# Kernel optimization log

Measured on AMD Instinct MI355X. Metric: run time of the kernel, lower is better.

The kernel has to match this reference:

```python
import jax, jax.numpy as jnp
import numpy as np

# Nemotron-H Mamba2 mixer decoder layer (prefill path, zero initial states,
# full context lengths). Dims per init_kwargs.
B, S, H = 1, 256, 4096
NH, P, G, N, K = 128, 64, 8, 128, 4   # num_heads, head_dim, n_groups, ssm_state_size, conv_kernel
D_INNER = NH * P                      # 8192
D_STATE = G * N                       # 1024
CONV_DIM = D_INNER + 2 * D_STATE      # 10240
IN_OUT = D_INNER + CONV_DIM + NH      # 18560
EPS = 1e-6


def setup_inputs() -> dict:
    key = jax.random.key(0)
    ks = jax.random.split(key, 8)
    sc = 0.02
    return {
        "hidden_states": jax.random.normal(ks[0], (B, S, H), jnp.float32),
        "conv_state": jnp.zeros((B, CONV_DIM, K - 1), jnp.float32),
        "ssm_state": jnp.zeros((B, NH, P, N), jnp.float32),
        "norm_weight": jnp.ones((H,), jnp.float32),
        "w_in": jax.random.normal(ks[1], (IN_OUT, H), jnp.float32) * sc,
        "conv_w": jax.random.normal(ks[2], (CONV_DIM, K), jnp.float32) * 0.2,
        "conv_b": jnp.zeros((CONV_DIM,), jnp.float32),
        "A_log": jax.random.uniform(ks[3], (NH,), jnp.float32, 0.0, 1.0),
        "D_param": jax.random.normal(ks[4], (NH,), jnp.float32) * 0.1,
        "dt_bias": jax.random.normal(ks[5], (NH,), jnp.float32) * 0.1,
        "ssm_norm_weight": jnp.ones((D_INNER,), jnp.float32),
        "w_out": jax.random.normal(ks[6], (H, D_INNER), jnp.float32) * sc,
    }


def _rmsnorm(x, w, eps=EPS):
    var = jnp.mean(x * x, axis=-1, keepdims=True)
    return x * jax.lax.rsqrt(var + eps) * w


def reference(hidden_states, conv_state, ssm_state, norm_weight, w_in, conv_w,
              conv_b, A_log, D_param, dt_bias, ssm_norm_weight, w_out):
    resid = hidden_states
    h = _rmsnorm(hidden_states, norm_weight)           # pre-mixer RMSNorm
    proj = jnp.einsum('bsh,oh->bso', h, w_in)          # in_proj [B,S,18560]
    gate = proj[..., :D_INNER]
    xconv = proj[..., D_INNER:D_INNER + CONV_DIM]
    dt = proj[..., D_INNER + CONV_DIM:]                # [B,S,NH]

    # depthwise causal conv1d, initial left context = conv_state
    xc = jnp.swapaxes(xconv, 1, 2)                     # [B,CONV_DIM,S]
    xpad = jnp.concatenate([conv_state, xc], axis=-1)  # [B,CONV_DIM,S+K-1]
    conv_state_out = xpad[:, :, -(K - 1):]
    y = conv_b[None, :, None]
    for j in range(K):                                 # K=4 taps, unrolled
        y = y + conv_w[:, j][None, :, None] * xpad[:, :, j:j + S]
    y = jax.nn.silu(jnp.swapaxes(y, 1, 2))             # [B,S,CONV_DIM]

    xs = y[..., :D_INNER].reshape(B, S, NH, P)
    Bs = y[..., D_INNER:D_INNER + D_STATE].reshape(B, S, G, N)
    Cs = y[..., D_INNER + D_STATE:].reshape(B, S, G, N)

    A = -jnp.exp(A_log)                                # [NH]
    dtp = jax.nn.softplus(dt + dt_bias)                # [B,S,NH]
    rep = NH // G
    Bh = jnp.repeat(Bs, rep, axis=2)                   # [B,S,NH,N]
    Ch = jnp.repeat(Cs, rep, axis=2)

    def step(state, inp):
        x_t, b_t, c_t, dt_t = inp                      # [B,NH,P],[B,NH,N],[B,NH,N],[B,NH]
        dA = jnp.exp(dt_t * A)                         # [B,NH]
        state = state * dA[..., None, None] + (dt_t[..., None] * x_t)[..., None] * b_t[:, :, None, :]
        y_t = jnp.einsum('bhpn,bhn->bhp', state, c_t)
        return state, y_t

    inps = (jnp.swapaxes(xs, 0, 1), jnp.swapaxes(Bh, 0, 1),
            jnp.swapaxes(Ch, 0, 1), jnp.swapaxes(dtp, 0, 1))
    ssm_state_out, ys = jax.lax.scan(step, ssm_state, inps)
    ys = jnp.swapaxes(ys, 0, 1) + D_param[None, None, :, None] * xs
    ssm_out = ys.reshape(B, S, D_INNER)

    # gated grouped RMSNorm (group_size = D_INNER // G = 1024)
    gated = ssm_out * jax.nn.silu(gate)
    gsize = D_INNER // G
    gg = gated.reshape(B, S, D_INNER // gsize, gsize)
    var = jnp.mean(gg * gg, axis=-1, keepdims=True)
    normed = (gg * jax.lax.rsqrt(var + EPS)).reshape(B, S, D_INNER) * ssm_norm_weight

    out = jnp.einsum('bsd,hd->bsh', normed, w_out)     # out_proj
    return resid + out, conv_state_out, ssm_state_out
```

## Files before the change

### kernel.cpp

```cpp
#include <hip/hip_runtime.h>
#include <hip/hip_bf16.h>

#define Sq 256
#define Hd 4096
#define NH 128
#define Pd 64
#define Gg 8
#define Nn 128
#define D_INNER 8192
#define D_STATE 1024
#define CONV_DIM 10240
#define IN_OUT 18560
#define DT_COL0 18432
#define EPSI 1e-6f

typedef _Float16 f16x8 __attribute__((ext_vector_type(8)));
typedef _Float16 f16x2 __attribute__((ext_vector_type(2)));
typedef float f32x4 __attribute__((ext_vector_type(4)));

__device__ inline ushort f2h(float f) {
  _Float16 h = (_Float16)f;
  return __builtin_bit_cast(ushort, h);
}
__device__ inline float h2f(ushort u) {
  return (float)__builtin_bit_cast(_Float16, u);
}
__device__ inline ushort f2h_lo(float f, ushort hi) {
  float hf = (float)__builtin_bit_cast(_Float16, hi);
  _Float16 l = (_Float16)(f - hf);
  return __builtin_bit_cast(ushort, l);
}
__device__ inline f16x2 pkrtz(float a, float b) {
  return __builtin_bit_cast(f16x2, __builtin_amdgcn_cvt_pkrtz(a, b));
}

__global__ __launch_bounds__(256) void rmsnorm_k(const float* __restrict__ x,
                                                 const float* __restrict__ w,
                                                 ushort* __restrict__ h_hi,
                                                 ushort* __restrict__ h_lo) {
  int s = blockIdx.x, t = threadIdx.x;
  const float4* row = reinterpret_cast<const float4*>(x + (size_t)s * Hd);
  const float4* wv  = reinterpret_cast<const float4*>(w);
  float4 v[4];
  float ss = 0.f;
#pragma unroll
  for (int i = 0; i < 4; i++) {
    v[i] = row[t + i * 256];
    ss += v[i].x * v[i].x + v[i].y * v[i].y + v[i].z * v[i].z + v[i].w * v[i].w;
  }
#pragma unroll
  for (int off = 32; off > 0; off >>= 1) ss += __shfl_xor(ss, off);
  __shared__ float red[4];
  if ((t & 63) == 0) red[t >> 6] = ss;
  __syncthreads();
  ss = red[0] + red[1] + red[2] + red[3];
  float scale = rsqrtf(ss * (1.f / (float)Hd) + EPSI);
  ushort4* hh = reinterpret_cast<ushort4*>(h_hi + (size_t)s * Hd);
  ushort4* hl = reinterpret_cast<ushort4*>(h_lo + (size_t)s * Hd);
#pragma unroll
  for (int i = 0; i < 4; i++) {
    float4 wi = wv[t + i * 256];
    float f0 = v[i].x * scale * wi.x, f1 = v[i].y * scale * wi.y;
    float f2 = v[i].z * scale * wi.z, f3 = v[i].w * scale * wi.w;
    ushort4 oh, ol;
    oh.x = f2h(f0); ol.x = f2h_lo(f0, oh.x);
    oh.y = f2h(f1); ol.y = f2h_lo(f1, oh.y);
    oh.z = f2h(f2); ol.z = f2h_lo(f2, oh.z);
    oh.w = f2h(f3); ol.w = f2h_lo(f3, oh.w);
    hh[t + i * 256] = oh;
    hl[t + i * 256] = ol;
  }
}

__global__ __launch_bounds__(256) void gemm_t128(const ushort* __restrict__ A,
                                                 const float* __restrict__ B,
                                                 float* __restrict__ C0,
                                                 ushort* __restrict__ Cp,
                                                 int ldc, int K, int kLen) {
  __shared__ __align__(16) ushort As[2][128 * 32];
  __shared__ __align__(16) ushort Bs[2][128 * 32];
  int t = threadIdx.x;
  int wave = t >> 6, lane = t & 63;
  int wr = wave >> 1, wc = wave & 1;
  int frow = lane & 15, gq = lane >> 4;
  int coltile = blockIdx.x >> 1;
  int rowBase = (blockIdx.x & 1) * 128;
  int bcol = coltile * 128;
  int z = blockIdx.z;
  int kStart = z * kLen;

  int ar = t >> 2;
  int ax = (ar >> 1) & 3;
  const ushort* ApG0 = A + (size_t)(rowBase + ar) * K + kStart + ((t & 3) ^ ax) * 8;
  const ushort* ApG1 = ApG0 + (size_t)64 * K;
  char* dstA0 = (char*)&As[0][0] + wave * 1024;
  char* dstA1 = (char*)&As[0][0] + 4096 + wave * 1024;

  int brow = t >> 1, bhalf = t & 1;
  int bx = (brow >> 1) & 3;
  const float* BpG = B + (size_t)(bcol + brow) * K + kStart + bhalf * 16;
  int bslot0 = ((2 * bhalf) ^ bx) * 16;
  int bslot1 = ((2 * bhalf + 1) ^ bx) * 16;
  float4 rb[4];

  f32x4 acc[4][4] = {};
  const int NT = kLen / 32;

#define ISSUE_B(kk) { _Pragma("unroll") for (int j = 0; j < 4; ++j) \
                        rb[j] = *(const float4*)(BpG + (kk) + j * 4); }
#define DMA_A(p, kk) { \
    __builtin_amdgcn_global_load_lds( \
        (const __attribute__((address_space(1))) void*)(ApG0 + (kk)), \
        (__attribute__((address_space(3))) void*)(dstA0 + (p) * 8192), 16, 0, 0); \
    __builtin_amdgcn_global_load_lds( \
        (const __attribute__((address_space(1))) void*)(ApG1 + (kk)), \
        (__attribute__((address_space(3))) void*)(dstA1 + (p) * 8192), 16, 0, 0); }
#define WRITE_B(p) { \
    union { f16x2 h2[8]; uint4 q[2]; } u; \
    u.h2[0] = pkrtz(rb[0].x, rb[0].y); u.h2[1] = pkrtz(rb[0].z, rb[0].w); \
    u.h2[2] = pkrtz(rb[1].x, rb[1].y); u.h2[3] = pkrtz(rb[1].z, rb[1].w); \
    u.h2[4] = pkrtz(rb[2].x, rb[2].y); u.h2[5] = pkrtz(rb[2].z, rb[2].w); \
    u.h2[6] = pkrtz(rb[3].x, rb[3].y); u.h2[7] = pkrtz(rb[3].z, rb[3].w); \
    char* bb = (char*)&Bs[0][0] + (p) * 8192 + brow * 64; \
    *(uint4*)(bb + bslot0) = u.q[0]; \
    *(uint4*)(bb + bslot1) = u.q[1]; }

  ISSUE_B(0)
  DMA_A(0, 0)
  WRITE_B(0)
  __syncthreads();

  for (int i = 0; i < NT; ++i) {
    int cur = i & 1;
    if (i + 1 < NT) {
      ISSUE_B((i + 1) * 32)
      DMA_A(cur ^ 1, (i + 1) * 32)
    }
    f16x8 af[4], bf[4];
#pragma unroll
    for (int m = 0; m < 4; ++m) {
      int row = wr * 64 + m * 16 + frow;
      af[m] = *(const f16x8*)((const char*)&As[0][0] + cur * 8192 + row * 64 +
                              ((gq ^ ((row >> 1) & 3)) * 16));
    }
#pragma unroll
    for (int n = 0; n < 4; ++n) {
      int row = wc * 64 + n * 16 + frow;
      bf[n] = *(const f16x8*)((const char*)&Bs[0][0] + cur * 8192 + row * 64 +
                              ((gq ^ ((row >> 1) & 3)) * 16));
    }
#pragma unroll
    for (int m = 0; m < 4; ++m)
#pragma unroll
      for (int n = 0; n < 4; ++n)
        acc[m][n] = __builtin_amdgcn_mfma_f32_16x16x32_f16(af[m], bf[n], acc[m][n], 0, 0, 0);
    __builtin_amdgcn_sched_barrier(0);
    if (i + 1 < NT) WRITE_B(cur ^ 1)
    __syncthreads();
  }
#undef ISSUE_B
#undef DMA_A
#undef WRITE_B

  if (z == 0) {
#pragma unroll
    for (int m = 0; m < 4; ++m) {
      int row0 = rowBase + wr * 64 + m * 16 + (lane >> 4) * 4;
#pragma unroll
      for (int n = 0; n < 4; ++n) {
        int col = bcol + wc * 64 + n * 16 + frow;
#pragma unroll
        for (int r = 0; r < 4; ++r)
          C0[(size_t)(row0 + r) * ldc + col] = acc[m][n][r];
      }
    }
  } else {
    ushort* Cz = Cp + (size_t)(z - 1) * Sq * ldc;
#pragma unroll
    for (int m = 0; m < 4; ++m) {
      int row0 = rowBase + wr * 64 + m * 16 + (lane >> 4) * 4;
#pragma unroll
      for (int n = 0; n < 4; ++n) {
        int col = bcol + wc * 64 + n * 16 + frow;
#pragma unroll
        for (int r = 0; r < 4; ++r)
          Cz[(size_t)(row0 + r) * ldc + col] = f2h(acc[m][n][r]);
      }
    }
  }
}

template<int BN, bool SPLIT>
__global__ __launch_bounds__(256) void gemm_mfma(const ushort* __restrict__ A_hi,
                                                 const ushort* __restrict__ A_lo,
                                                 const float* __restrict__ B,
                                                 float* __restrict__ C,
                                                 int ldc, int K, int kLen,
                                                 int bcol0, int M) {
  constexpr int BK = 64;
  constexpr int LDA = 72;
  constexpr int N_REP = BN / 32;
  constexpr int BQN = (BN == 128) ? 8 : 4;
  __shared__ __align__(16) ushort As[64 * LDA];
  __shared__ __align__(16) ushort Bs[BN * LDA];
  __shared__ __align__(16) ushort AsL[SPLIT ? 64 * LDA : 1];
  __shared__ __align__(16) ushort BsL[SPLIT ? BN * LDA : 1];

  int t = threadIdx.x;
  int wave = t >> 6, lane = t & 63;
  int wr = wave >> 1, wc = wave & 1;
  int frow = lane & 15, fk = (lane >> 4) * 8;
  int rowBase = blockIdx.x * 64;
  int bcol = bcol0 + blockIdx.y * BN;
  int ccol = blockIdx.y * BN;
  int kStart = blockIdx.z * kLen;
  C += (size_t)blockIdx.z * M * ldc;

  int arow = t >> 2, ak = (t & 3) * 16;
  const ushort* Ap  = A_hi + (size_t)(rowBase + arow) * K + ak;
  const ushort* ApL = SPLIT ? (A_lo + (size_t)(rowBase + arow) * K + ak) : nullptr;

  int brow, bq;
  if constexpr (BN == 128) { brow = t >> 1; bq = (t & 1) * 32; }
  else                     { brow = t >> 2; bq = (t & 3) * 16; }
  const float* Bp = B + (size_t)(bcol + brow) * K + bq;

  f32x4 acc[2][N_REP] = {};
  uint4 aPre[2], aPreL[2];
  float4 bPre[BQN];

  auto loadK = [&](int kk) {
    aPre[0] = *reinterpret_cast<const uint4*>(Ap + kk);
    aPre[1] = *reinterpret_cast<const uint4*>(Ap + kk + 8);
    if constexpr (SPLIT) {
      aPreL[0] = *reinterpret_cast<const uint4*>(ApL + kk);
      aPreL[1] = *reinterpret_cast<const uint4*>(ApL + kk + 8);
    }
#pragma unroll
    for (int j = 0; j < BQN; ++j)
      bPre[j] = *reinterpret_cast<const float4*>(Bp + kk + j * 4);
  };

  loadK(kStart);
  for (int ki = 0; ki < kLen; ki += BK) {
    __syncthreads();
    *reinterpret_cast<uint4*>(&As[arow * LDA + ak])     = aPre[0];
    *reinterpret_cast<uint4*>(&As[arow * LDA + ak + 8]) = aPre[1];
    if constexpr (SPLIT) {
      *reinterpret_cast<uint4*>(&AsL[arow * LDA + ak])     = aPreL[0];
      *reinterpret_cast<uint4*>(&AsL[arow * LDA + ak + 8]) = aPreL[1];
    }
    {
      ushort hb[BQN * 4];
      ushort lb[SPLIT ? BQN * 4 : 1];
      const float* bf = reinterpret_cast<const float*>(bPre);
#pragma unroll
      for (int j = 0; j < BQN * 4; ++j) {
        hb[j] = f2h(bf[j]);
        if constexpr (SPLIT) lb[j] = f2h_lo(bf[j], hb[j]);
      }
#pragma unroll
      for (int j = 0; j < BQN / 2; ++j)
        *reinterpret_cast<uint4*>(&Bs[brow * LDA + bq + j * 8]) =
            reinterpret_cast<const uint4*>(hb)[j];
      if constexpr (SPLIT) {
#pragma unroll
        for (int j = 0; j < BQN / 2; ++j)
          *reinterpret_cast<uint4*>(&BsL[brow * LDA + bq + j * 8]) =
              reinterpret_cast<const uint4*>(lb)[j];
      }
    }
    __syncthreads();
    if (ki + BK < kLen) loadK(kStart + ki + BK);
    f16x8 af[2][2], bfv[N_REP][2];
    f16x8 afL[SPLIT ? 2 : 1][2], bfL[SPLIT ? N_REP : 1][2];
#pragma unroll
    for (int m = 0; m < 2; ++m)
#pragma unroll
      for (int kh = 0; kh < 2; ++kh) {
        af[m][kh] = *reinterpret_cast<const f16x8*>(
            &As[(wr * 32 + m * 16 + frow) * LDA + kh * 32 + fk]);
        if constexpr (SPLIT)
          afL[m][kh] = *reinterpret_cast<const f16x8*>(
              &AsL[(wr * 32 + m * 16 + frow) * LDA + kh * 32 + fk]);
      }
#pragma unroll
    for (int n = 0; n < N_REP; ++n)
#pragma unroll
      for (int kh = 0; kh < 2; ++kh) {
        bfv[n][kh] = *reinterpret_cast<const f16x8*>(
            &Bs[(wc * (BN / 2) + n * 16 + frow) * LDA + kh * 32 + fk]);
        if constexpr (SPLIT)
          bfL[n][kh] = *reinterpret_cast<const f16x8*>(
              &BsL[(wc * (BN / 2) + n * 16 + frow) * LDA + kh * 32 + fk]);
      }
#pragma unroll
    for (int kh = 0; kh < 2; ++kh)
#pragma unroll
      for (int m = 0; m < 2; ++m)
#pragma unroll
        for (int n = 0; n < N_REP; ++n) {
          acc[m][n] = __builtin_amdgcn_mfma_f32_16x16x32_f16(af[m][kh], bfv[n][kh], acc[m][n], 0, 0, 0);
          if constexpr (SPLIT) {
            acc[m][n] = __builtin_amdgcn_mfma_f32_16x16x32_f16(af[m][kh], bfL[n][kh], acc[m][n], 0, 0, 0);
            acc[m][n] = __builtin_amdgcn_mfma_f32_16x16x32_f16(afL[m][kh], bfv[n][kh], acc[m][n], 0, 0, 0);
          }
        }
  }

#pragma unroll
  for (int m = 0; m < 2; ++m) {
    int row0 = rowBase + wr * 32 + m * 16 + (lane >> 4) * 4;
#pragma unroll
    for (int n = 0; n < N_REP; ++n) {
      int col = ccol + wc * (BN / 2) + n * 16 + frow;
#pragma unroll
      for (int r = 0; r < 4; ++r)
        C[(size_t)(row0 + r) * ldc + col] = acc[m][n][r];
    }
  }
}

__global__ __launch_bounds__(256) void reduce_in_k(float* __restrict__ proj,
                                                   const ushort* __restrict__ pp) {
  int i = blockIdx.x * 256 + threadIdx.x;
  const size_t PL = (size_t)Sq * IN_OUT;
  float4 o = reinterpret_cast<const float4*>(proj)[i];
#pragma unroll
  for (int zz = 0; zz < 3; ++zz) {
    ushort4 hv = reinterpret_cast<const ushort4*>(pp + zz * PL)[i];
    o.x += h2f(hv.x); o.y += h2f(hv.y); o.z += h2f(hv.z); o.w += h2f(hv.w);
  }
  reinterpret_cast<float4*>(proj)[i] = o;
}

__global__ __launch_bounds__(256) void conv_silu_k(const float* __restrict__ proj,
                                                   const float* __restrict__ cstate,
                                                   const float* __restrict__ cw,
                                                   const float* __restrict__ cb,
                                                   float* __restrict__ y) {
  int c = blockIdx.x * 256 + threadIdx.x;
  int s = blockIdx.y;
  float acc = cb[c];
  float4 w4 = *reinterpret_cast<const float4*>(cw + c * 4);
  float wj[4] = {w4.x, w4.y, w4.z, w4.w};
#pragma unroll
  for (int j = 0; j < 4; j++) {
    int si = s + j - 3;
    float v = (si < 0) ? cstate[c * 3 + (si + 3)]
                       : proj[(size_t)si * IN_OUT + D_INNER + c];
    acc += wj[j] * v;
  }
  float sig = 1.f / (1.f + expf(-acc));
  y[(size_t)s * CONV_DIM + c] = acc * sig;
}

__global__ __launch_bounds__(256) void conv_state_out_k(const float* __restrict__ proj,
                                                        float* __restrict__ out1) {
  int idx = blockIdx.x * 256 + threadIdx.x;
  int c = idx / 3, tt = idx % 3;
  out1[idx] = proj[(size_t)(Sq - 3 + tt) * IN_OUT + D_INNER + c];
}

__global__ __launch_bounds__(256) void dt_k(const float* __restrict__ dtfix,
                                            const float* __restrict__ dt_bias,
                                            float* __restrict__ dtp) {
  int idx = blockIdx.x * 256 + threadIdx.x;
  int hh = idx & 127;
  float v = dtfix[idx] + dtfix[32768 + idx] + dtfix[65536 + idx] + dtfix[98304 + idx]
            + dt_bias[hh];
  dtp[idx] = (v > 20.f) ? v : log1pf(expf(v));
}

#define CS 16
__global__ __launch_bounds__(256) void ssm_scan_k(const float* __restrict__ y_conv,
                                                  const float* __restrict__ dtp,
                                                  const float* __restrict__ sstate_in,
                                                  const float* __restrict__ A_log,
                                                  const float* __restrict__ D_param,
                                                  float* __restrict__ ys_out,
                                                  float* __restrict__ sstate_out) {
  int h = blockIdx.x >> 1;
  int pb = (blockIdx.x & 1) * 32;
  int t = threadIdx.x;
  int ng = t & 7, pl = t >> 3;
  int g = h >> 4;
  float A = -expf(A_log[h]);
  float Dp = D_param[h];

  float st[16];
  {
    const float* sp = sstate_in + ((size_t)h * Pd + pb + pl) * Nn + ng * 16;
#pragma unroll
    for (int i = 0; i < 16; i += 4) {
      float4 v = *reinterpret_cast<const float4*>(sp + i);
      st[i] = v.x; st[i + 1] = v.y; st[i + 2] = v.z; st[i + 3] = v.w;
    }
  }

  __shared__ float ybuf[CS][296];
  __shared__ float dts[CS];
  int lr = t >> 4;
  int lc = t & 15;

  for (int ch = 0; ch < Sq / CS; ++ch) {
    int s0 = ch * CS;
    __syncthreads();
    const float* rowp = y_conv + (size_t)(s0 + lr) * CONV_DIM;
#pragma unroll
    for (int j = 0; j < 5; ++j) {
      int c = lc + 16 * j;
      if (c < 72) {
        const float* src;
        if (c < 8)       src = rowp + h * 64 + pb + c * 4;
        else if (c < 40) src = rowp + D_INNER + g * 128 + (c - 8) * 4;
        else             src = rowp + D_INNER + D_STATE + g * 128 + (c - 40) * 4;
        *reinterpret_cast<float4*>(&ybuf[lr][c * 4]) = *reinterpret_cast<const float4*>(src);
      }
    }
    if (t < CS) dts[t] = dtp[(s0 + t) * NH + h];
    __syncthreads();

#pragma unroll 4
    for (int stp = 0; stp < CS; ++stp) {
      float dt = dts[stp];
      float dA = expf(dt * A);
      float x0 = ybuf[stp][pl];
      float dtx = dt * x0;
      float y0 = 0.f;
#pragma unroll
      for (int i = 0; i < 16; ++i) {
        float b = ybuf[stp][32 + ng * 16 + i];
        float c = ybuf[stp][160 + ng * 16 + i];
        st[i] = st[i] * dA + dtx * b;
        y0 += st[i] * c;
      }
      y0 += __shfl_xor(y0, 1); y0 += __shfl_xor(y0, 2); y0 += __shfl_xor(y0, 4);
      if (ng == 0)
        ys_out[(size_t)(s0 + stp) * D_INNER + h * 64 + pb + pl] = y0 + Dp * x0;
    }
  }

  float* so = sstate_out + ((size_t)h * Pd + pb + pl) * Nn + ng * 16;
#pragma unroll
  for (int i = 0; i < 16; i += 4)
    *reinterpret_cast<float4*>(so + i) = make_float4(st[i], st[i + 1], st[i + 2], st[i + 3]);
}

__global__ __launch_bounds__(256) void gated_norm_k(const float* __restrict__ ys,
                                                    const float* __restrict__ proj,
                                                    const float* __restrict__ w,
                                                    ushort* __restrict__ out_h) {
  int s = blockIdx.x, g = blockIdx.y, t = threadIdx.x;
  float vals[4];
  float ss = 0.f;
#pragma unroll
  for (int i = 0; i < 4; i++) {
    int d = g * 1024 + i * 256 + t;
    float gate = proj[(size_t)s * IN_OUT + d];
    float v = ys[(size_t)s * D_INNER + d] * (gate / (1.f + expf(-gate)));
    vals[i] = v;
    ss += v * v;
  }
#pragma unroll
  for (int off = 32; off > 0; off >>= 1) ss += __shfl_xor(ss, off);
  __shared__ float red[4];
  if ((t & 63) == 0) red[t >> 6] = ss;
  __syncthreads();
  ss = red[0] + red[1] + red[2] + red[3];
  float scale = rsqrtf(ss * (1.f / 1024.f) + EPSI);
#pragma unroll
  for (int i = 0; i < 4; i++) {
    int d = g * 1024 + i * 256 + t;
    out_h[(size_t)s * D_INNER + d] = f2h(vals[i] * scale * w[d]);
  }
}

__global__ __launch_bounds__(256) void reduce_out_k(const float* __restrict__ p0,
                                                    const ushort* __restrict__ pph,
                                                    const float* __restrict__ hidden,
                                                    float* __restrict__ out0) {
  int i = blockIdx.x * 256 + threadIdx.x;
  const size_t PL = (size_t)Sq * Hd;
  float4 o = reinterpret_cast<const float4*>(hidden)[i];
  float4 a = reinterpret_cast<const float4*>(p0)[i];
  o.x += a.x; o.y += a.y; o.z += a.z; o.w += a.w;
#pragma unroll
  for (int zz = 0; zz < 15; ++zz) {
    ushort4 hv = reinterpret_cast<const ushort4*>(pph + zz * PL)[i];
    o.x += h2f(hv.x); o.y += h2f(hv.y); o.z += h2f(hv.z); o.w += h2f(hv.w);
  }
  reinterpret_cast<float4*>(out0)[i] = o;
}

extern "C" void kernel_launch(void* const* d_in, const int* in_sizes, int n_in,
                              void* d_out, int out_size, void* d_ws, size_t ws_size,
                              hipStream_t stream) {
  const float* hidden    = (const float*)d_in[0];
  const float* cstate_in = (const float*)d_in[1];
  const float* sstate_in = (const float*)d_in[2];
  const float* norm_w    = (const float*)d_in[3];
  const float* w_in      = (const float*)d_in[4];
  const float* conv_w    = (const float*)d_in[5];
  const float* conv_b    = (const float*)d_in[6];
  const float* A_log     = (const float*)d_in[7];
  const float* D_param   = (const float*)d_in[8];
  const float* dt_bias   = (const float*)d_in[9];
  const float* ssm_nw    = (const float*)d_in[10];
  const float* w_out     = (const float*)d_in[11];

  float* out0 = (float*)d_out;
  float* out1 = out0 + (size_t)Sq * Hd;
  float* out2 = out1 + (size_t)CONV_DIM * 3;

  ushort* h_hi  = (ushort*)d_ws;
  ushort* h_lo  = h_hi + (size_t)Sq * Hd;
  float*  proj  = (float*)(h_lo + (size_t)Sq * Hd);
  ushort* pp_in = (ushort*)(proj + (size_t)Sq * IN_OUT);
  float*  y_conv = (float*)pp_in;
  float*  dtp   = y_conv + (size_t)Sq * CONV_DIM;
  float*  ys    = dtp + (size_t)Sq * NH;
  ushort* ys_h  = (ushort*)(ys + (size_t)Sq * D_INNER);
  float*  dtfix = (float*)(ys_h + (size_t)Sq * D_INNER);
  float*  op0    = (float*)d_ws;
  ushort* pp_out = (ushort*)(op0 + (size_t)Sq * Hd);

  rmsnorm_k<<<Sq, 256, 0, stream>>>(hidden, norm_w, h_hi, h_lo);
  gemm_t128<<<dim3(2 * (IN_OUT / 128), 1, 4), 256, 0, stream>>>(
      h_hi, w_in, proj, pp_in, IN_OUT, Hd, Hd / 4);
  reduce_in_k<<<(Sq * IN_OUT / 4) / 256, 256, 0, stream>>>(proj, pp_in);
  gemm_mfma<64, true><<<dim3(4, 2, 4), 256, 0, stream>>>(
      h_hi, h_lo, w_in, dtfix, NH, Hd, Hd / 4, DT_COL0, Sq);
  conv_silu_k<<<dim3(CONV_DIM / 256, Sq), 256, 0, stream>>>(proj, cstate_in, conv_w, conv_b, y_conv);
  conv_state_out_k<<<(CONV_DIM * 3) / 256, 256, 0, stream>>>(proj, out1);
  dt_k<<<(Sq * NH) / 256, 256, 0, stream>>>(dtfix, dt_bias, dtp);
  ssm_scan_k<<<NH * 2, 256, 0, stream>>>(y_conv, dtp, sstate_in, A_log, D_param, ys, out2);
  gated_norm_k<<<dim3(Sq, Gg), 256, 0, stream>>>(ys, proj, ssm_nw, ys_h);
  gemm_t128<<<dim3(2 * (Hd / 128), 1, 16), 256, 0, stream>>>(
      ys_h, w_out, op0, pp_out, Hd, D_INNER, D_INNER / 16);
  reduce_out_k<<<(Sq * Hd / 4) / 256, 256, 0, stream>>>(op0, pp_out, hidden, out0);
}
```

Measured before the change: 370.1 us.

## Triple-buffer GEMM LDS tiles with two-stage prefetch and manual vmcnt waits

Expands the GEMM's shared-memory staging from double to triple buffering and prefetches the A and B tiles two K-steps ahead, alternating between two register sets for B. Explicit s_waitcnt vmcnt/lgkmcnt waits and raw s_barrier replace __syncthreads, so loads for later steps stay in flight across the barrier. The goal is to hide global-memory latency behind the MFMA work. In exchange it uses more LDS and registers, which can lower occupancy, and it assumes NT is even and relies on hand-counted vmcnt values.

```diff
diff --git a/kernel.cpp b/kernel.cpp
--- a/kernel.cpp
+++ b/kernel.cpp
@@ -77,8 +77,8 @@
                                                  float* __restrict__ C0,
                                                  ushort* __restrict__ Cp,
                                                  int ldc, int K, int kLen) {
-  __shared__ __align__(16) ushort As[2][128 * 32];
-  __shared__ __align__(16) ushort Bs[2][128 * 32];
+  __shared__ __align__(16) ushort As[3][128 * 32];
+  __shared__ __align__(16) ushort Bs[3][128 * 32];
   int t = threadIdx.x;
   int wave = t >> 6, lane = t & 63;
   int wr = wave >> 1, wc = wave & 1;
@@ -101,13 +101,15 @@
   const float* BpG = B + (size_t)(bcol + brow) * K + kStart + bhalf * 16;
   int bslot0 = ((2 * bhalf) ^ bx) * 16;
   int bslot1 = ((2 * bhalf + 1) ^ bx) * 16;
-  float4 rb[4];
+  float4 rb0[4], rb1[4];
 
   f32x4 acc[4][4] = {};
   const int NT = kLen / 32;
 
-#define ISSUE_B(kk) { _Pragma("unroll") for (int j = 0; j < 4; ++j) \
-                        rb[j] = *(const float4*)(BpG + (kk) + j * 4); }
+#define ISSUE_B0(kk) { _Pragma("unroll") for (int j = 0; j < 4; ++j) \
+                         rb0[j] = *(const float4*)(BpG + (kk) + j * 4); }
+#define ISSUE_B1(kk) { _Pragma("unroll") for (int j = 0; j < 4; ++j) \
+                         rb1[j] = *(const float4*)(BpG + (kk) + j * 4); }
 #define DMA_A(p, kk) { \
     __builtin_amdgcn_global_load_lds( \
         (const __attribute__((address_space(1))) void*)(ApG0 + (kk)), \
@@ -115,52 +117,64 @@
     __builtin_amdgcn_global_load_lds( \
         (const __attribute__((address_space(1))) void*)(ApG1 + (kk)), \
         (__attribute__((address_space(3))) void*)(dstA1 + (p) * 8192), 16, 0, 0); }
-#define WRITE_B(p) { \
+#define WRITE_B(p, rbv) { \
     union { f16x2 h2[8]; uint4 q[2]; } u; \
-    u.h2[0] = pkrtz(rb[0].x, rb[0].y); u.h2[1] = pkrtz(rb[0].z, rb[0].w); \
-    u.h2[2] = pkrtz(rb[1].x, rb[1].y); u.h2[3] = pkrtz(rb[1].z, rb[1].w); \
-    u.h2[4] = pkrtz(rb[2].x, rb[2].y); u.h2[5] = pkrtz(rb[2].z, rb[2].w); \
-    u.h2[6] = pkrtz(rb[3].x, rb[3].y); u.h2[7] = pkrtz(rb[3].z, rb[3].w); \
+    u.h2[0] = pkrtz(rbv[0].x, rbv[0].y); u.h2[1] = pkrtz(rbv[0].z, rbv[0].w); \
+    u.h2[2] = pkrtz(rbv[1].x, rbv[1].y); u.h2[3] = pkrtz(rbv[1].z, rbv[1].w); \
+    u.h2[4] = pkrtz(rbv[2].x, rbv[2].y); u.h2[5] = pkrtz(rbv[2].z, rbv[2].w); \
+    u.h2[6] = pkrtz(rbv[3].x, rbv[3].y); u.h2[7] = pkrtz(rbv[3].z, rbv[3].w); \
     char* bb = (char*)&Bs[0][0] + (p) * 8192 + brow * 64; \
     *(uint4*)(bb + bslot0) = u.q[0]; \
     *(uint4*)(bb + bslot1) = u.q[1]; }
-
-  ISSUE_B(0)
+#define COMPUTE(p) { \
+    f16x8 af[4], bf[4]; \
+    _Pragma("unroll") for (int m = 0; m < 4; ++m) { \
+      int row = wr * 64 + m * 16 + frow; \
+      af[m] = *(const f16x8*)((const char*)&As[0][0] + (p) * 8192 + row * 64 + \
+                              ((gq ^ ((row >> 1) & 3)) * 16)); } \
+    _Pragma("unroll") for (int n = 0; n < 4; ++n) { \
+      int row = wc * 64 + n * 16 + frow; \
+      bf[n] = *(const f16x8*)((const char*)&Bs[0][0] + (p) * 8192 + row * 64 + \
+                              ((gq ^ ((row >> 1) & 3)) * 16)); } \
+    _Pragma("unroll") for (int m = 0; m < 4; ++m) \
+      _Pragma("unroll") for (int n = 0; n < 4; ++n) \
+        acc[m][n] = __builtin_amdgcn_mfma_f32_16x16x32_f16(af[m], bf[n], acc[m][n], 0, 0, 0); }
+#define SB() __builtin_amdgcn_sched_barrier(0)
+#define BARRIER() { asm volatile("s_waitcnt lgkmcnt(0)" ::: "memory"); SB(); \
+                    __builtin_amdgcn_s_barrier(); SB(); }
+#define STEP(ii, IM, RBW) { \
+    int p  = (ii) % 3, pn = ((ii) + 1) % 3, pf = ((ii) + 2) % 3; \
+    if ((ii) + 2 < NT) { IM(((ii) + 2) * 32); DMA_A(pf, ((ii) + 2) * 32); } \
+    COMPUTE(p); \
+    SB(); \
+    if ((ii) + 1 < NT) { WRITE_B(pn, RBW); } \
+    if ((ii) + 2 < NT) { asm volatile("s_waitcnt vmcnt(6)" ::: "memory"); } \
+    else               { asm volatile("s_waitcnt vmcnt(0)" ::: "memory"); } \
+    SB(); \
+    BARRIER(); \
+    (void)pn; (void)pf; }
+
+  ISSUE_B0(0)
   DMA_A(0, 0)
-  WRITE_B(0)
-  __syncthreads();
-
-  for (int i = 0; i < NT; ++i) {
-    int cur = i & 1;
-    if (i + 1 < NT) {
-      ISSUE_B((i + 1) * 32)
-      DMA_A(cur ^ 1, (i + 1) * 32)
-    }
-    f16x8 af[4], bf[4];
-#pragma unroll
-    for (int m = 0; m < 4; ++m) {
-      int row = wr * 64 + m * 16 + frow;
-      af[m] = *(const f16x8*)((const char*)&As[0][0] + cur * 8192 + row * 64 +
-                              ((gq ^ ((row >> 1) & 3)) * 16));
-    }
-#pragma unroll
-    for (int n = 0; n < 4; ++n) {
-      int row = wc * 64 + n * 16 + frow;
-      bf[n] = *(const f16x8*)((const char*)&Bs[0][0] + cur * 8192 + row * 64 +
-                              ((gq ^ ((row >> 1) & 3)) * 16));
-    }
-#pragma unroll
-    for (int m = 0; m < 4; ++m)
-#pragma unroll
-      for (int n = 0; n < 4; ++n)
-        acc[m][n] = __builtin_amdgcn_mfma_f32_16x16x32_f16(af[m], bf[n], acc[m][n], 0, 0, 0);
-    __builtin_amdgcn_sched_barrier(0);
-    if (i + 1 < NT) WRITE_B(cur ^ 1)
-    __syncthreads();
-  }
-#undef ISSUE_B
+  ISSUE_B1(32)
+  DMA_A(1, 32)
+  WRITE_B(0, rb0)
+  asm volatile("s_waitcnt vmcnt(6)" ::: "memory");
+  SB();
+  BARRIER();
+
+  for (int i = 0; i < NT; i += 2) {
+    STEP(i,     ISSUE_B0, rb1)
+    STEP(i + 1, ISSUE_B1, rb0)
+  }
+#undef ISSUE_B0
+#undef ISSUE_B1
 #undef DMA_A
 #undef WRITE_B
+#undef COMPUTE
+#undef SB
+#undef BARRIER
+#undef STEP
 
   if (z == 0) {
 #pragma unroll
```

Result: no change. 374.4 us (+1.1%).
